# Kernel tuning notes

Measured on AMD Instinct MI355X. Metric: run time of the kernel, lower is better.

## Reference

```python
import jax, jax.numpy as jnp
import numpy as np

B, D, H, W, T, C = 2, 16, 16, 16, 16, 96
NH = 4                      # num_heads
WS = (4, 4, 4, 4)           # window size
SS = (2, 2, 2, 2)           # shift size
EPS = 1e-5
HIDDEN = 4 * C


def _compute_mask():
    # Standard Swin shifted-window attention mask, extended to 4D.
    img = np.zeros((D, H, W, T), np.float32)
    sl = [[slice(0, -WS[i]), slice(-WS[i], -SS[i]), slice(-SS[i], None)] for i in range(4)]
    cnt = 0
    for a in sl[0]:
        for b in sl[1]:
            for c in sl[2]:
                for d in sl[3]:
                    img[a, b, c, d] = cnt
                    cnt += 1
    x = img.reshape(D // WS[0], WS[0], H // WS[1], WS[1], W // WS[2], WS[2], T // WS[3], WS[3])
    x = x.transpose(0, 2, 4, 6, 1, 3, 5, 7).reshape(-1, WS[0] * WS[1] * WS[2] * WS[3])
    diff = x[:, None, :] - x[:, :, None]
    return np.where(diff != 0, np.float32(-100.0), np.float32(0.0))


def setup_inputs() -> dict:
    key = jax.random.key(0)
    ks = jax.random.split(key, 6)
    w = lambda k, shape: jax.random.normal(k, shape, jnp.float32) * 0.02
    return {
        'x': jax.random.normal(ks[0], (B, D, H, W, T, C), jnp.float32),
        'mask_matrix': jnp.asarray(_compute_mask()),
        'norm1_g': jnp.ones((C,), jnp.float32), 'norm1_b': jnp.zeros((C,), jnp.float32),
        'qkv_w': w(ks[1], (3 * C, C)), 'qkv_b': jnp.zeros((3 * C,), jnp.float32),
        'proj_w': w(ks[2], (C, C)), 'proj_b': jnp.zeros((C,), jnp.float32),
        'norm2_g': jnp.ones((C,), jnp.float32), 'norm2_b': jnp.zeros((C,), jnp.float32),
        'fc1_w': w(ks[3], (HIDDEN, C)), 'fc1_b': jnp.zeros((HIDDEN,), jnp.float32),
        'fc2_w': w(ks[4], (C, HIDDEN)), 'fc2_b': jnp.zeros((C,), jnp.float32),
    }


def _ln(x, g, b):
    mu = jnp.mean(x, -1, keepdims=True)
    var = jnp.var(x, -1, keepdims=True)
    return (x - mu) * jax.lax.rsqrt(var + EPS) * g + b


def _partition(x):
    # (B, D, H, W, T, C) -> (B*nw, N, C)
    b, c = x.shape[0], x.shape[-1]
    x = x.reshape(b, D // WS[0], WS[0], H // WS[1], WS[1], W // WS[2], WS[2], T // WS[3], WS[3], c)
    x = x.transpose(0, 1, 3, 5, 7, 2, 4, 6, 8, 9)
    return x.reshape(-1, WS[0] * WS[1] * WS[2] * WS[3], c)


def _reverse(win, b):
    c = win.shape[-1]
    x = win.reshape(b, D // WS[0], H // WS[1], W // WS[2], T // WS[3], WS[0], WS[1], WS[2], WS[3], c)
    x = x.transpose(0, 1, 5, 2, 6, 3, 7, 4, 8, 9)
    return x.reshape(b, D, H, W, T, c)


def reference(x, mask_matrix, norm1_g, norm1_b, qkv_w, qkv_b, proj_w, proj_b,
              norm2_g, norm2_b, fc1_w, fc1_b, fc2_w, fc2_b):
    b, c = x.shape[0], x.shape[-1]
    hd = c // NH
    scale = hd ** -0.5
    shortcut = x
    # norm -> (no pad needed: dims divisible by window) -> cyclic shift
    xn = _ln(x, norm1_g, norm1_b)
    xs = jnp.roll(xn, shift=(-SS[0], -SS[1], -SS[2], -SS[3]), axis=(1, 2, 3, 4))
    win = _partition(xs)                              # (B_, N, C)
    B_, N, _ = win.shape
    qkv = (win @ qkv_w.T + qkv_b).reshape(B_, N, 3, NH, hd).transpose(2, 0, 3, 1, 4)
    q, k, v = qkv[0] * scale, qkv[1], qkv[2]          # (B_, NH, N, hd)
    attn = jnp.einsum('bhid,bhjd->bhij', q, k)        # (B_, NH, N, N)
    nw = mask_matrix.shape[0]
    attn = attn.reshape(B_ // nw, nw, NH, N, N) + mask_matrix[None, :, None]
    attn = jax.nn.softmax(attn.reshape(B_, NH, N, N), axis=-1)
    out = jnp.einsum('bhij,bhjd->bhid', attn, v)
    out = out.transpose(0, 2, 1, 3).reshape(B_, N, c)
    out = out @ proj_w.T + proj_b
    xr = _reverse(out, b)
    xr = jnp.roll(xr, shift=SS, axis=(1, 2, 3, 4))    # reverse cyclic shift
    x = shortcut + xr
    # MLP block
    h = _ln(x, norm2_g, norm2_b)
    h = jax.nn.gelu(h @ fc1_w.T + fc1_b, approximate=False)
    return x + (h @ fc2_w.T + fc2_b)
```

## Files before the change

kernel.cpp:

```cpp
#include <hip/hip_runtime.h>

#define TOK   131072
#define BWIN  512

typedef __attribute__((ext_vector_type(8))) short bf16x8;
typedef __attribute__((ext_vector_type(4))) short bf16x4;
typedef __attribute__((ext_vector_type(4))) float f32x4;

__device__ __forceinline__ unsigned short f2us(float f) {
  union { float f; unsigned int i; } x; x.f = f;
  return (unsigned short)((x.i + 0x7fffu + ((x.i >> 16) & 1u)) >> 16);
}
__device__ __forceinline__ unsigned cvtpk(float lo, float hi) {
  unsigned r;
  asm("v_cvt_pk_bf16_f32 %0, %1, %2" : "=v"(r) : "v"(lo), "v"(hi));
  return r;
}
union U8 { uint2 u; bf16x4 v; };

#define IW1   0
#define IW2   36864
#define IQKV  73728
#define IPROJ 104448
#define IMG_SHORTS 113664

__global__ __launch_bounds__(256) void k_prepw(
    const float* __restrict__ fc1_w, const float* __restrict__ fc2_w,
    const float* __restrict__ qkv_w, const float* __restrict__ proj_w,
    unsigned short* __restrict__ img) {
  int i = blockIdx.x * 256 + threadIdx.x;
  const int l = (i >> 3) & 63, j = i & 7;
  const int quad = l >> 4, l15 = l & 15;
  float v = 0.f;
  if (i < 36864) {
    int f = i >> 9; int nc = f / 18, rem = f - nc * 18;
    int ks = rem / 6, nt = rem - ks * 6;
    v = fc1_w[(size_t)(nc * 96 + nt * 16 + l15) * 96 + ks * 32 + quad * 8 + j];
  } else if (i < 73728) {
    int f = (i - 36864) >> 9; int nc = f / 18, rem = f - nc * 18;
    int ks = rem / 6, nt = rem - ks * 6;
    v = fc2_w[(size_t)(nt * 16 + l15) * 384 + nc * 96 + ks * 32 + quad * 8 + j];
  } else if (i < 104448) {
    int f = (i - 73728) >> 9; int h = f / 15, rem = f - h * 15;
    int ks = rem / 5, mt = rem - ks * 5;
    int e = mt * 16 + l15;
    if (e < 72) {
      int grp = e / 24, rr = e - grp * 24;
      v = qkv_w[(size_t)(grp * 96 + h * 24 + rr) * 96 + ks * 32 + quad * 8 + j];
    }
  } else {
    int f = (i - 104448) >> 9; int ks = f / 6, nt = f - ks * 6;
    v = proj_w[(size_t)(nt * 16 + l15) * 96 + ks * 32 + quad * 8 + j];
  }
  img[i] = f2us(v);
}

__global__ __launch_bounds__(256) void k_ln1(const float* __restrict__ x,
                                             const float* __restrict__ g,
                                             const float* __restrict__ b,
                                             unsigned short* __restrict__ xn) {
  const int r = threadIdx.x >> 1, hf = threadIdx.x & 1;
  const int t = blockIdx.x * 128 + r;
  const int b_ = t >> 8, n = t & 255;
  const int batch = b_ >> 8, wi = b_ & 255;
  const int wd = (wi >> 6) & 3, wh = (wi >> 4) & 3, ww = (wi >> 2) & 3, wt = wi & 3;
  const int aa = (n >> 6) & 3, bb = (n >> 4) & 3, cc = (n >> 2) & 3, dd = n & 3;
  const int sd = (wd * 4 + aa + 2) & 15, sh = (wh * 4 + bb + 2) & 15;
  const int sw = (ww * 4 + cc + 2) & 15, st = (wt * 4 + dd + 2) & 15;
  const size_t gg = ((((size_t)(batch * 16 + sd) * 16 + sh) * 16 + sw) * 16 + st);

  const float4* base = (const float4*)(x + gg * 96 + hf * 48);
  float v[48];
  float s = 0.f, q2 = 0.f;
  #pragma unroll
  for (int j = 0; j < 12; j++) {
    float4 f = base[j];
    v[4 * j] = f.x; v[4 * j + 1] = f.y; v[4 * j + 2] = f.z; v[4 * j + 3] = f.w;
    s += f.x + f.y + f.z + f.w;
    q2 += f.x * f.x + f.y * f.y + f.z * f.z + f.w * f.w;
  }
  s += __shfl_xor(s, 1); q2 += __shfl_xor(q2, 1);
  const float mu = s * (1.f / 96.f);
  const float var = q2 * (1.f / 96.f) - mu * mu;
  const float rs = rsqrtf(fmaxf(var, 0.f) + 1e-5f);
  unsigned int* row = (unsigned int*)xn + (size_t)t * 48 + hf * 24;
  #pragma unroll
  for (int jj = 0; jj < 24; jj++) {
    int k0 = hf * 48 + 2 * jj;
    float a0 = (v[2 * jj]     - mu) * rs * g[k0]     + b[k0];
    float a1 = (v[2 * jj + 1] - mu) * rs * g[k0 + 1] + b[k0 + 1];
    row[jj] = cvtpk(a0, a1);
  }
}

__global__ __launch_bounds__(256, 2) void k_win(
    const unsigned short* __restrict__ xn,
    const unsigned short* __restrict__ img,
    const float* __restrict__ qkv_b,
    unsigned short* __restrict__ og) {
  __shared__ __align__(16) short s_k[256 * 36];
  __shared__ __align__(16) short s_vt[32 * 260];
  __shared__ unsigned char s_lb[256];

  const int tid = threadIdx.x;
  const int w = tid >> 6, l = tid & 63, quad = l >> 4, l15 = l & 15;
  const int q0 = w * 64;
  const int b_ = blockIdx.x;
  const int wi = b_ & 255;
  const int wd = (wi >> 6) & 3, wh = (wi >> 4) & 3, ww = (wi >> 2) & 3, wt = wi & 3;
  const float scale = 0.20412414523193154f;
  const f32x4 fz = {0.f, 0.f, 0.f, 0.f};

  {
    const int n = tid;
    const int aa = (n >> 6) & 3, bb = (n >> 4) & 3, cc = (n >> 2) & 3, dd = n & 3;
    const int p0 = wd * 4 + aa, p1 = wh * 4 + bb, p2 = ww * 4 + cc, p3 = wt * 4 + dd;
    const int r0 = p0 >= 14 ? 2 : (p0 >= 12 ? 1 : 0);
    const int r1 = p1 >= 14 ? 2 : (p1 >= 12 ? 1 : 0);
    const int r2 = p2 >= 14 ? 2 : (p2 >= 12 ? 1 : 0);
    const int r3 = p3 >= 14 ? 2 : (p3 >= 12 ? 1 : 0);
    s_lb[n] = (unsigned char)(((r0 * 3 + r1) * 3 + r2) * 3 + r3);
    *(uint2*)&s_k[n * 36 + 24] = make_uint2(0u, 0u);
    *(uint2*)&s_k[n * 36 + 28] = make_uint2(0u, 0u);
    unsigned int* vz = (unsigned int*)(s_vt + 24 * 260);
    for (int i = tid; i < 8 * 130; i += 256) vz[i] = 0u;
  }
  __syncthreads();

  const unsigned short* xw = xn + (size_t)b_ * 256 * 96;
  const unsigned short* wq = img + IQKV;

  for (int h = 0; h < 4; h++) {
    f32x4 acc[5][4];
    #pragma unroll
    for (int mt = 0; mt < 5; mt++)
      #pragma unroll
      for (int nt = 0; nt < 4; nt++) acc[mt][nt] = fz;
    #pragma unroll
    for (int ks = 0; ks < 3; ks++) {
      bf16x8 aw[5];
      #pragma unroll
      for (int mt = 0; mt < 5; mt++)
        aw[mt] = *(const bf16x8*)(wq + ((h * 3 + ks) * 5 + mt) * 512 + l * 8);
      #pragma unroll
      for (int nt = 0; nt < 4; nt++) {
        bf16x8 bx = *(const bf16x8*)(xw + (size_t)(q0 + nt * 16 + l15) * 96 + ks * 32 + quad * 8);
        #pragma unroll
        for (int mt = 0; mt < 5; mt++)
          acc[mt][nt] = __builtin_amdgcn_mfma_f32_16x16x32_bf16(aw[mt], bx, acc[mt][nt], 0, 0, 0);
      }
    }
    U8 qq[2][4];
    #pragma unroll
    for (int mt = 0; mt < 2; mt++) {
      const int e0 = mt * 16 + quad * 4;
      float b0 = qkv_b[h * 24 + e0],     b1 = qkv_b[h * 24 + e0 + 1];
      float b2 = qkv_b[h * 24 + e0 + 2], b3 = qkv_b[h * 24 + e0 + 3];
      #pragma unroll
      for (int nt = 0; nt < 4; nt++) {
        qq[mt][nt].u.x = cvtpk((acc[mt][nt][0] + b0) * scale, (acc[mt][nt][1] + b1) * scale);
        qq[mt][nt].u.y = cvtpk((acc[mt][nt][2] + b2) * scale, (acc[mt][nt][3] + b3) * scale);
      }
    }
    #pragma unroll
    for (int mt = 1; mt < 5; mt++) {
      const int e0 = mt * 16 + quad * 4;
      #pragma unroll
      for (int nt = 0; nt < 4; nt++) {
        const int tok = q0 + nt * 16 + l15;
        if (e0 >= 24 && e0 < 48) {
          const int e = e0 - 24;
          uint2 pk;
          pk.x = cvtpk(acc[mt][nt][0] + qkv_b[96 + h * 24 + e],
                       acc[mt][nt][1] + qkv_b[96 + h * 24 + e + 1]);
          pk.y = cvtpk(acc[mt][nt][2] + qkv_b[96 + h * 24 + e + 2],
                       acc[mt][nt][3] + qkv_b[96 + h * 24 + e + 3]);
          *(uint2*)&s_k[tok * 36 + e] = pk;
        } else if (e0 >= 48 && e0 < 72) {
          const int e = e0 - 48;
          #pragma unroll
          for (int r = 0; r < 4; r++)
            s_vt[(e + r) * 260 + tok] = (short)f2us(acc[mt][nt][r] + qkv_b[192 + h * 24 + e + r]);
        }
      }
    }
    __syncthreads();
    #pragma unroll 1
    for (int mt4 = 0; mt4 < 4; mt4++) {
      const int qt0 = q0 + mt4 * 16;
      f32x4 sc[16];
      #pragma unroll
      for (int km = 0; km < 16; km++) sc[km] = fz;
      const bf16x4 bq0 = qq[0][mt4].v, bq1 = qq[1][mt4].v;
      __builtin_amdgcn_s_setprio(1);
      #pragma unroll
      for (int km = 0; km < 16; km++) {
        bf16x4 ak0 = *(const bf16x4*)&s_k[(km * 16 + l15) * 36 + quad * 4];
        bf16x4 ak1 = *(const bf16x4*)&s_k[(km * 16 + l15) * 36 + 16 + quad * 4];
        sc[km] = __builtin_amdgcn_mfma_f32_16x16x16bf16_1k(ak0, bq0, sc[km], 0, 0, 0);
        sc[km] = __builtin_amdgcn_mfma_f32_16x16x16bf16_1k(ak1, bq1, sc[km], 0, 0, 0);
      }
      __builtin_amdgcn_s_setprio(0);
      const unsigned lq = s_lb[qt0 + l15];
      float rsum = 0.f;
      #pragma unroll
      for (int km = 0; km < 16; km++) {
        unsigned lj = *(const unsigned*)&s_lb[km * 16 + quad * 4];
        float p0 = ((lj & 255u)         == lq) ? __expf(sc[km][0]) : 0.f;
        float p1 = (((lj >> 8) & 255u)  == lq) ? __expf(sc[km][1]) : 0.f;
        float p2 = (((lj >> 16) & 255u) == lq) ? __expf(sc[km][2]) : 0.f;
        float p3 = ((lj >> 24)          == lq) ? __expf(sc[km][3]) : 0.f;
        sc[km][0] = p0; sc[km][1] = p1; sc[km][2] = p2; sc[km][3] = p3;
        rsum += (p0 + p1) + (p2 + p3);
      }
      rsum += __shfl_xor(rsum, 16, 64);
      rsum += __shfl_xor(rsum, 32, 64);
      const float inv = 1.f / rsum;
      f32x4 ov0 = fz, ov1 = fz;
      __builtin_amdgcn_s_setprio(1);
      #pragma unroll
      for (int km = 0; km < 16; km++) {
        U8 bp;
        bp.u.x = cvtpk(sc[km][0], sc[km][1]);
        bp.u.y = cvtpk(sc[km][2], sc[km][3]);
        bf16x4 av0 = *(const bf16x4*)&s_vt[l15 * 260 + km * 16 + quad * 4];
        bf16x4 av1 = *(const bf16x4*)&s_vt[(16 + l15) * 260 + km * 16 + quad * 4];
        ov0 = __builtin_amdgcn_mfma_f32_16x16x16bf16_1k(av0, bp.v, ov0, 0, 0, 0);
        ov1 = __builtin_amdgcn_mfma_f32_16x16x16bf16_1k(av1, bp.v, ov1, 0, 0, 0);
      }
      __builtin_amdgcn_s_setprio(0);
      uint2 o0, o1;
      o0.x = cvtpk(ov0[0] * inv, ov0[1] * inv);
      o0.y = cvtpk(ov0[2] * inv, ov0[3] * inv);
      o1.x = cvtpk(ov1[0] * inv, ov1[1] * inv);
      o1.y = cvtpk(ov1[2] * inv, ov1[3] * inv);
      size_t ob = ((size_t)b_ * 256 + qt0 + l15) * 96 + h * 24;
      *(uint2*)&og[ob + quad * 4] = o0;
      if (quad < 2) *(uint2*)&og[ob + 16 + quad * 4] = o1;
    }
    __syncthreads();
  }
}

__global__ __launch_bounds__(256, 2) void k_pm(
    const unsigned short* __restrict__ og, const float* __restrict__ x,
    const unsigned short* __restrict__ img,
    const float* __restrict__ proj_b,
    const float* __restrict__ n2g, const float* __restrict__ n2b,
    const float* __restrict__ fc1_b, const float* __restrict__ fc2_b,
    float* __restrict__ out) {
  __shared__ __align__(16) short s_a[128 * 104];
  __shared__ __align__(16) short s_h[128 * 104];

  const int tid = threadIdx.x;
  const int w = tid >> 6, l = tid & 63, quad = l >> 4, l15 = l & 15;
  const int t0 = blockIdx.x * 128;
  const f32x4 fz = {0.f, 0.f, 0.f, 0.f};

  float gn[6], bn[6], pb[6], f2[6];
  #pragma unroll
  for (int nt = 0; nt < 6; nt++) {
    int c = nt * 16 + l15;
    gn[nt] = n2g[c]; bn[nt] = n2b[c]; pb[nt] = proj_b[c]; f2[nt] = fc2_b[c];
  }

  f32x4 pacc[2][6];
  #pragma unroll
  for (int m = 0; m < 2; m++)
    #pragma unroll
    for (int nt = 0; nt < 6; nt++) pacc[m][nt] = fz;
  #pragma unroll
  for (int ks = 0; ks < 3; ks++) {
    bf16x8 bw[6];
    #pragma unroll
    for (int nt = 0; nt < 6; nt++)
      bw[nt] = *(const bf16x8*)(img + IPROJ + (ks * 6 + nt) * 512 + l * 8);
    #pragma unroll
    for (int m = 0; m < 2; m++) {
      bf16x8 af = *(const bf16x8*)(og + (size_t)(t0 + w * 32 + m * 16 + l15) * 96 + ks * 32 + quad * 8);
      #pragma unroll
      for (int nt = 0; nt < 6; nt++)
        pacc[m][nt] = __builtin_amdgcn_mfma_f32_16x16x32_bf16(af, bw[nt], pacc[m][nt], 0, 0, 0);
    }
  }

  float x2[2][6][4];
  size_t gg[2][4];
  #pragma unroll
  for (int m = 0; m < 2; m++) {
    #pragma unroll
    for (int r = 0; r < 4; r++) {
      const int T = t0 + w * 32 + m * 16 + quad * 4 + r;
      const int b_ = T >> 8, n = T & 255;
      const int batch = b_ >> 8, wi = b_ & 255;
      const int wd = (wi >> 6) & 3, wh = (wi >> 4) & 3, ww = (wi >> 2) & 3, wt = wi & 3;
      const int aa = (n >> 6) & 3, bb = (n >> 4) & 3, cc = (n >> 2) & 3, dd = n & 3;
      const int sd = (wd * 4 + aa + 2) & 15, sh = (wh * 4 + bb + 2) & 15;
      const int sw = (ww * 4 + cc + 2) & 15, st = (wt * 4 + dd + 2) & 15;
      gg[m][r] = ((((size_t)(batch * 16 + sd) * 16 + sh) * 16 + sw) * 16 + st);
      float s = 0.f, q = 0.f;
      #pragma unroll
      for (int nt = 0; nt < 6; nt++) {
        float v = x[gg[m][r] * 96 + nt * 16 + l15] + pb[nt] + pacc[m][nt][r];
        x2[m][nt][r] = v;
        s += v; q += v * v;
      }
      s += __shfl_xor(s, 1); q += __shfl_xor(q, 1);
      s += __shfl_xor(s, 2); q += __shfl_xor(q, 2);
      s += __shfl_xor(s, 4); q += __shfl_xor(q, 4);
      s += __shfl_xor(s, 8); q += __shfl_xor(q, 8);
      const float mu = s * (1.f / 96.f);
      const float var = q * (1.f / 96.f) - mu * mu;
      const float rs = rsqrtf(fmaxf(var, 0.f) + 1e-5f);
      const int tr = w * 32 + m * 16 + quad * 4 + r;
      #pragma unroll
      for (int nt = 0; nt < 6; nt++)
        s_a[tr * 104 + nt * 16 + l15] =
            (short)f2us((x2[m][nt][r] - mu) * rs * gn[nt] + bn[nt]);
    }
  }

  f32x4 acc2[2][6];
  #pragma unroll
  for (int m = 0; m < 2; m++)
    #pragma unroll
    for (int i = 0; i < 6; i++) acc2[m][i] = fz;

  for (int nc = 0; nc < 4; nc++) {
    f32x4 acc1[2][6];
    #pragma unroll
    for (int m = 0; m < 2; m++)
      #pragma unroll
      for (int i = 0; i < 6; i++) acc1[m][i] = fz;
    #pragma unroll
    for (int ks = 0; ks < 3; ks++) {
      bf16x8 bw[6];
      #pragma unroll
      for (int nt = 0; nt < 6; nt++)
        bw[nt] = *(const bf16x8*)(img + IW1 + ((nc * 3 + ks) * 6 + nt) * 512 + l * 8);
      #pragma unroll
      for (int m = 0; m < 2; m++) {
        bf16x8 af = *(const bf16x8*)&s_a[(w * 32 + m * 16 + l15) * 104 + ks * 32 + quad * 8];
        #pragma unroll
        for (int nt = 0; nt < 6; nt++)
          acc1[m][nt] = __builtin_amdgcn_mfma_f32_16x16x32_bf16(af, bw[nt], acc1[m][nt], 0, 0, 0);
      }
    }
    #pragma unroll
    for (int m = 0; m < 2; m++)
      #pragma unroll
      for (int nt = 0; nt < 6; nt++) {
        int col = nt * 16 + l15;
        float bv = fc1_b[nc * 96 + col];
        #pragma unroll
        for (int r = 0; r < 4; r++) {
          float z = acc1[m][nt][r] + bv;
          float g = 0.5f * z * (1.f + erff(z * 0.70710678118654752f));
          s_h[(w * 32 + m * 16 + quad * 4 + r) * 104 + col] = (short)f2us(g);
        }
      }
    #pragma unroll
    for (int ks = 0; ks < 3; ks++) {
      bf16x8 bw[6];
      #pragma unroll
      for (int nt = 0; nt < 6; nt++)
        bw[nt] = *(const bf16x8*)(img + IW2 + ((nc * 3 + ks) * 6 + nt) * 512 + l * 8);
      #pragma unroll
      for (int m = 0; m < 2; m++) {
        bf16x8 af = *(const bf16x8*)&s_h[(w * 32 + m * 16 + l15) * 104 + ks * 32 + quad * 8];
        #pragma unroll
        for (int nt = 0; nt < 6; nt++)
          acc2[m][nt] = __builtin_amdgcn_mfma_f32_16x16x32_bf16(af, bw[nt], acc2[m][nt], 0, 0, 0);
      }
    }
  }

  #pragma unroll
  for (int m = 0; m < 2; m++)
    #pragma unroll
    for (int r = 0; r < 4; r++)
      #pragma unroll
      for (int nt = 0; nt < 6; nt++)
        out[gg[m][r] * 96 + nt * 16 + l15] = x2[m][nt][r] + acc2[m][nt][r] + f2[nt];
}

extern "C" void kernel_launch(void* const* d_in, const int* in_sizes, int n_in,
                              void* d_out, int out_size, void* d_ws, size_t ws_size,
                              hipStream_t stream) {
  const float* x      = (const float*)d_in[0];
  const float* n1g    = (const float*)d_in[2];
  const float* n1b    = (const float*)d_in[3];
  const float* qkv_w  = (const float*)d_in[4];
  const float* qkv_b  = (const float*)d_in[5];
  const float* proj_w = (const float*)d_in[6];
  const float* proj_b = (const float*)d_in[7];
  const float* n2g    = (const float*)d_in[8];
  const float* n2b    = (const float*)d_in[9];
  const float* fc1_w  = (const float*)d_in[10];
  const float* fc1_b  = (const float*)d_in[11];
  const float* fc2_w  = (const float*)d_in[12];
  const float* fc2_b  = (const float*)d_in[13];
  float* out = (float*)d_out;

  char* ws = (char*)d_ws;
  unsigned short* xn  = (unsigned short*)ws;
  unsigned short* img = (unsigned short*)(ws + 25165824u);
  unsigned short* og  = (unsigned short*)(ws + 25165824u + 227328u);

  k_prepw<<<IMG_SHORTS / 256, 256, 0, stream>>>(fc1_w, fc2_w, qkv_w, proj_w, img);
  k_ln1<<<TOK / 128, 256, 0, stream>>>(x, n1g, n1b, xn);
  k_win<<<BWIN, 256, 0, stream>>>(xn, img, qkv_b, og);
  k_pm<<<TOK / 128, 256, 0, stream>>>(og, x, img, proj_b, n2g, n2b, fc1_b, fc2_b, out);
}
```

Before: 299.3 us.

## Fuse LayerNorm1 into window attention kernel and use fast erf approximation for GELU

Removes the separate k_ln1 kernel. Each k_win thread now loads its tokens' fp32 rows straight from x, with the shifted-window gather done inline. It computes LayerNorm with cross-lane shuffles and keeps the normalized bf16 MFMA operands in registers for all four heads. This drops one launch and the bf16 xn round trip through global memory, in exchange for more registers in k_win. Separately, erff in the MLP GELU is replaced by an Abramowitz-Stegun polynomial using hardware rcp and exp, which lowers accuracy slightly.

```diff
diff --git a/kernel.cpp b/kernel.cpp
--- a/kernel.cpp
+++ b/kernel.cpp
@@ -17,6 +17,18 @@
   return r;
 }
 union U8 { uint2 u; bf16x4 v; };
+union B8 { bf16x8 v; unsigned u[4]; };
+
+__device__ __forceinline__ float gelu_f(float z) {
+  const float u = fabsf(z) * 0.70710678118654752f;
+  float t;
+  asm("v_rcp_f32 %0, %1" : "=v"(t) : "v"(fmaf(0.3275911f, u, 1.f)));
+  float poly = t * (0.254829592f + t * (-0.284496736f + t * (1.421413741f +
+               t * (-1.453152027f + t * 1.061405429f))));
+  float er = 1.f - poly * __expf(-u * u);
+  er = copysignf(er, z);
+  return 0.5f * z * (1.f + er);
+}
 
 #define IW1   0
 #define IW2   36864
@@ -55,47 +67,10 @@
   img[i] = f2us(v);
 }
 
-__global__ __launch_bounds__(256) void k_ln1(const float* __restrict__ x,
-                                             const float* __restrict__ g,
-                                             const float* __restrict__ b,
-                                             unsigned short* __restrict__ xn) {
-  const int r = threadIdx.x >> 1, hf = threadIdx.x & 1;
-  const int t = blockIdx.x * 128 + r;
-  const int b_ = t >> 8, n = t & 255;
-  const int batch = b_ >> 8, wi = b_ & 255;
-  const int wd = (wi >> 6) & 3, wh = (wi >> 4) & 3, ww = (wi >> 2) & 3, wt = wi & 3;
-  const int aa = (n >> 6) & 3, bb = (n >> 4) & 3, cc = (n >> 2) & 3, dd = n & 3;
-  const int sd = (wd * 4 + aa + 2) & 15, sh = (wh * 4 + bb + 2) & 15;
-  const int sw = (ww * 4 + cc + 2) & 15, st = (wt * 4 + dd + 2) & 15;
-  const size_t gg = ((((size_t)(batch * 16 + sd) * 16 + sh) * 16 + sw) * 16 + st);
-
-  const float4* base = (const float4*)(x + gg * 96 + hf * 48);
-  float v[48];
-  float s = 0.f, q2 = 0.f;
-  #pragma unroll
-  for (int j = 0; j < 12; j++) {
-    float4 f = base[j];
-    v[4 * j] = f.x; v[4 * j + 1] = f.y; v[4 * j + 2] = f.z; v[4 * j + 3] = f.w;
-    s += f.x + f.y + f.z + f.w;
-    q2 += f.x * f.x + f.y * f.y + f.z * f.z + f.w * f.w;
-  }
-  s += __shfl_xor(s, 1); q2 += __shfl_xor(q2, 1);
-  const float mu = s * (1.f / 96.f);
-  const float var = q2 * (1.f / 96.f) - mu * mu;
-  const float rs = rsqrtf(fmaxf(var, 0.f) + 1e-5f);
-  unsigned int* row = (unsigned int*)xn + (size_t)t * 48 + hf * 24;
-  #pragma unroll
-  for (int jj = 0; jj < 24; jj++) {
-    int k0 = hf * 48 + 2 * jj;
-    float a0 = (v[2 * jj]     - mu) * rs * g[k0]     + b[k0];
-    float a1 = (v[2 * jj + 1] - mu) * rs * g[k0 + 1] + b[k0 + 1];
-    row[jj] = cvtpk(a0, a1);
-  }
-}
-
 __global__ __launch_bounds__(256, 2) void k_win(
-    const unsigned short* __restrict__ xn,
+    const float* __restrict__ x,
     const unsigned short* __restrict__ img,
+    const float* __restrict__ n1g, const float* __restrict__ n1b,
     const float* __restrict__ qkv_b,
     unsigned short* __restrict__ og) {
   __shared__ __align__(16) short s_k[256 * 36];
@@ -106,7 +81,7 @@
   const int w = tid >> 6, l = tid & 63, quad = l >> 4, l15 = l & 15;
   const int q0 = w * 64;
   const int b_ = blockIdx.x;
-  const int wi = b_ & 255;
+  const int batch = b_ >> 8, wi = b_ & 255;
   const int wd = (wi >> 6) & 3, wh = (wi >> 4) & 3, ww = (wi >> 2) & 3, wt = wi & 3;
   const float scale = 0.20412414523193154f;
   const f32x4 fz = {0.f, 0.f, 0.f, 0.f};
@@ -125,9 +100,58 @@
     unsigned int* vz = (unsigned int*)(s_vt + 24 * 260);
     for (int i = tid; i < 8 * 130; i += 256) vz[i] = 0u;
   }
+
+  B8 bx[4][3];
+  {
+    float gch[24], bch[24];
+    #pragma unroll
+    for (int ks = 0; ks < 3; ks++) {
+      float4 g0 = *(const float4*)(n1g + ks * 32 + quad * 8);
+      float4 g1 = *(const float4*)(n1g + ks * 32 + quad * 8 + 4);
+      float4 b0 = *(const float4*)(n1b + ks * 32 + quad * 8);
+      float4 b1 = *(const float4*)(n1b + ks * 32 + quad * 8 + 4);
+      gch[ks*8+0]=g0.x; gch[ks*8+1]=g0.y; gch[ks*8+2]=g0.z; gch[ks*8+3]=g0.w;
+      gch[ks*8+4]=g1.x; gch[ks*8+5]=g1.y; gch[ks*8+6]=g1.z; gch[ks*8+7]=g1.w;
+      bch[ks*8+0]=b0.x; bch[ks*8+1]=b0.y; bch[ks*8+2]=b0.z; bch[ks*8+3]=b0.w;
+      bch[ks*8+4]=b1.x; bch[ks*8+5]=b1.y; bch[ks*8+6]=b1.z; bch[ks*8+7]=b1.w;
+    }
+    #pragma unroll
+    for (int nt = 0; nt < 4; nt++) {
+      const int tok = q0 + nt * 16 + l15;
+      const int aa = (tok >> 6) & 3, bb = (tok >> 4) & 3, cc = (tok >> 2) & 3, dd = tok & 3;
+      const int sd = (wd * 4 + aa + 2) & 15, sh_ = (wh * 4 + bb + 2) & 15;
+      const int sw_ = (ww * 4 + cc + 2) & 15, st_ = (wt * 4 + dd + 2) & 15;
+      const size_t gg = ((((size_t)(batch * 16 + sd) * 16 + sh_) * 16 + sw_) * 16 + st_);
+      const float* xp = x + gg * 96 + quad * 8;
+      float v[24];
+      float s = 0.f, q = 0.f;
+      #pragma unroll
+      for (int ks = 0; ks < 3; ks++) {
+        float4 f0 = *(const float4*)(xp + ks * 32);
+        float4 f1 = *(const float4*)(xp + ks * 32 + 4);
+        v[ks*8+0]=f0.x; v[ks*8+1]=f0.y; v[ks*8+2]=f0.z; v[ks*8+3]=f0.w;
+        v[ks*8+4]=f1.x; v[ks*8+5]=f1.y; v[ks*8+6]=f1.z; v[ks*8+7]=f1.w;
+        s += (f0.x + f0.y) + (f0.z + f0.w) + (f1.x + f1.y) + (f1.z + f1.w);
+        q += f0.x*f0.x + f0.y*f0.y + f0.z*f0.z + f0.w*f0.w
+           + f1.x*f1.x + f1.y*f1.y + f1.z*f1.z + f1.w*f1.w;
+      }
+      s += __shfl_xor(s, 16, 64); q += __shfl_xor(q, 16, 64);
+      s += __shfl_xor(s, 32, 64); q += __shfl_xor(q, 32, 64);
+      const float mu = s * (1.f / 96.f);
+      const float var = q * (1.f / 96.f) - mu * mu;
+      const float rs = rsqrtf(fmaxf(var, 0.f) + 1e-5f);
+      #pragma unroll
+      for (int ks = 0; ks < 3; ks++)
+        #pragma unroll
+        for (int jj = 0; jj < 4; jj++) {
+          const int c = ks * 8 + 2 * jj;
+          bx[nt][ks].u[jj] = cvtpk((v[c]     - mu) * rs * gch[c]     + bch[c],
+                                   (v[c + 1] - mu) * rs * gch[c + 1] + bch[c + 1]);
+        }
+    }
+  }
   __syncthreads();
 
-  const unsigned short* xw = xn + (size_t)b_ * 256 * 96;
   const unsigned short* wq = img + IQKV;
 
   for (int h = 0; h < 4; h++) {
@@ -144,10 +168,10 @@
         aw[mt] = *(const bf16x8*)(wq + ((h * 3 + ks) * 5 + mt) * 512 + l * 8);
       #pragma unroll
       for (int nt = 0; nt < 4; nt++) {
-        bf16x8 bx = *(const bf16x8*)(xw + (size_t)(q0 + nt * 16 + l15) * 96 + ks * 32 + quad * 8);
+        const bf16x8 bxv = bx[nt][ks].v;
         #pragma unroll
         for (int mt = 0; mt < 5; mt++)
-          acc[mt][nt] = __builtin_amdgcn_mfma_f32_16x16x32_bf16(aw[mt], bx, acc[mt][nt], 0, 0, 0);
+          acc[mt][nt] = __builtin_amdgcn_mfma_f32_16x16x32_bf16(aw[mt], bxv, acc[mt][nt], 0, 0, 0);
       }
     }
     U8 qq[2][4];
@@ -355,8 +379,7 @@
         #pragma unroll
         for (int r = 0; r < 4; r++) {
           float z = acc1[m][nt][r] + bv;
-          float g = 0.5f * z * (1.f + erff(z * 0.70710678118654752f));
-          s_h[(w * 32 + m * 16 + quad * 4 + r) * 104 + col] = (short)f2us(g);
+          s_h[(w * 32 + m * 16 + quad * 4 + r) * 104 + col] = (short)f2us(gelu_f(z));
         }
       }
     #pragma unroll
@@ -403,12 +426,10 @@
   float* out = (float*)d_out;
 
   char* ws = (char*)d_ws;
-  unsigned short* xn  = (unsigned short*)ws;
-  unsigned short* img = (unsigned short*)(ws + 25165824u);
-  unsigned short* og  = (unsigned short*)(ws + 25165824u + 227328u);
+  unsigned short* img = (unsigned short*)ws;
+  unsigned short* og  = (unsigned short*)(ws + 227328u);
 
   k_prepw<<<IMG_SHORTS / 256, 256, 0, stream>>>(fc1_w, fc2_w, qkv_w, proj_w, img);
-  k_ln1<<<TOK / 128, 256, 0, stream>>>(x, n1g, n1b, xn);
-  k_win<<<BWIN, 256, 0, stream>>>(xn, img, qkv_b, og);
+  k_win<<<BWIN, 256, 0, stream>>>(x, img, n1g, n1b, qkv_b, og);
   k_pm<<<TOK / 128, 256, 0, stream>>>(og, x, img, proj_b, n2g, n2b, fc1_b, fc2_b, out);
 }
```

After: 284.5 us. 4.9% less time.
